# Optimization experiments

Measured on AMD Instinct MI355X. Metric: run time of the kernel, lower is better.

Reference implementation:

```python
import jax, jax.numpy as jnp
import numpy as np

S, B, H = 1024, 4096, 8  # seq_len, batch, hidden (=input) size


def setup_inputs() -> dict:
    key = jax.random.key(0)
    k0, k1, k2, k3, k4 = jax.random.split(key, 5)
    scale = 1.0 / np.sqrt(H)  # matches torch uniform(-1/sqrt(H), 1/sqrt(H)) magnitude
    return {
        "input_": jax.random.normal(k0, (S, B, H), dtype=jnp.float32),
        "w_ih": jax.random.uniform(k1, (3 * H, H), jnp.float32, -scale, scale),
        "w_hh": jax.random.uniform(k2, (3 * H, H), jnp.float32, -scale, scale),
        "b_ih": jax.random.uniform(k3, (3 * H,), jnp.float32, -scale, scale),
        "b_hh": jax.random.uniform(k4, (3 * H,), jnp.float32, -scale, scale),
    }


def _gru_seq(input_, w_ih, w_hh, b_ih, b_hh):
    # Precompute input-side gate projections for all timesteps in one GEMM:
    # (S, B, 3H); gate order in PyTorch GRU is r, z, n.
    xg = jnp.einsum("sbi,gi->sbg", input_, w_ih) + b_ih
    h0 = jnp.zeros((input_.shape[1], w_hh.shape[1]), dtype=input_.dtype)

    def step(h, xg_t):
        hg = h @ w_hh.T + b_hh                      # (B, 3H)
        xr, xz, xn = jnp.split(xg_t, 3, axis=-1)
        hr, hz, hn = jnp.split(hg, 3, axis=-1)
        r = jax.nn.sigmoid(xr + hr)
        z = jax.nn.sigmoid(xz + hz)
        n = jnp.tanh(xn + r * hn)
        h_new = (1.0 - z) * n + z * h
        return h_new, h_new

    h_last, outputs = jax.lax.scan(step, h0, xg)
    return outputs, h_last[None]  # (S, B, H), (1, B, H) like torch GRU


def reference(input_, w_ih, w_hh, b_ih, b_hh):
    return _gru_seq(input_, w_ih, w_hh, b_ih, b_hh)
```

## Files before the change

kernel.cpp:

```cpp
#include <hip/hip_runtime.h>

#define SS 1024
#define BB 4096
#define HH 8
#define XSTRIDE (BB * HH)

__device__ __forceinline__ int dpp_x1(int v) { return __builtin_amdgcn_mov_dpp(v, 0xB1, 0xF, 0xF, true); }
__device__ __forceinline__ int dpp_x2(int v) { return __builtin_amdgcn_mov_dpp(v, 0x4E, 0xF, 0xF, true); }
__device__ __forceinline__ int dpp_x3(int v) { return __builtin_amdgcn_mov_dpp(v, 0x1B, 0xF, 0xF, true); }
__device__ __forceinline__ int dpp_x7(int v) { return __builtin_amdgcn_mov_dpp(v, 0x141, 0xF, 0xF, true); }
__device__ __forceinline__ int dpp_r8(int v) { return __builtin_amdgcn_mov_dpp(v, 0x128, 0xF, 0xF, true); }

#define ALOADD(DST, PTR) asm volatile("global_load_dword %0, %1, off" : "=v"(DST) : "v"(PTR))

#define WAITV(N) do {                                                                  \
    asm volatile("s_waitcnt vmcnt(" #N ")" ::: "memory");                              \
    __builtin_amdgcn_sched_barrier(0);                                                 \
} while (0)

#define XFULL(BUF, V) do {                                                             \
    const float va = BUF[V];                                                           \
    const int vai = __float_as_int(va);                                                \
    const float vb = __int_as_float(dpp_x1(vai));                                      \
    const float vc = __int_as_float(dpp_x2(vai));                                      \
    const float vd = __int_as_float(dpp_x3(vai));                                      \
    float sr0 = fmaf(va, wri[0], bias_rx); sr0 = fmaf(vb, wri[1], sr0);                \
    float sr1 = vc * wri[2];               sr1 = fmaf(vd, wri[3], sr1);                \
    float sz0 = fmaf(va, wzi[0], bias_zx); sz0 = fmaf(vb, wzi[1], sz0);                \
    float sz1 = vc * wzi[2];               sz1 = fmaf(vd, wzi[3], sz1);                \
    float sn0 = fmaf(va, wni[0], bias_nx); sn0 = fmaf(vb, wni[1], sn0);                \
    float sn1 = vc * wni[2];               sn1 = fmaf(vd, wni[3], sn1);                \
    const float srt = sr0 + sr1, szt = sz0 + sz1, snt = sn0 + sn1;                     \
    xr[V] = srt + __int_as_float(dpp_r8(__float_as_int(srt)));                         \
    xz[V] = szt + __int_as_float(dpp_r8(__float_as_int(szt)));                         \
    xn[V] = snt + __int_as_float(dpp_r8(__float_as_int(snt)));                         \
} while (0)

#define GROUP(BUF, SBASE) do {                                                         \
    XFULL(BUF, 0);                                                                     \
    XFULL(BUF, 1);                                                                     \
    _Pragma("unroll")                                                                  \
    for (int u = 0; u < 8; ++u) {                                                      \
                                        \
        const int hvi = __float_as_int(hv);                                            \
        const float ha = hv;                                                           \
        const float hbv = __int_as_float(dpp_x1(hvi));                                 \
        const float hc = __int_as_float(dpp_x2(hvi));                                  \
        const float hd = __int_as_float(dpp_x3(hvi));                                  \
        float pr0 = ha * wrh[0];               pr0 = fmaf(hbv, wrh[1], pr0);           \
        float pr1 = hc * wrh[2];               pr1 = fmaf(hd, wrh[3], pr1);            \
        float pz0 = ha * wzh[0];               pz0 = fmaf(hbv, wzh[1], pz0);           \
        float pz1 = hc * wzh[2];               pz1 = fmaf(hd, wzh[3], pz1);            \
        float pn0 = fmaf(ha, wnh[0], bias_nh); pn0 = fmaf(hbv, wnh[1], pn0);           \
        float pn1 = hc * wnh[2];               pn1 = fmaf(hd, wnh[3], pn1);            \
        const float prt = pr0 + pr1, pzt = pz0 + pz1, pnt = pn0 + pn1;                 \
        const float srr = xr[u] + (prt + __int_as_float(dpp_r8(__float_as_int(prt)))); \
        const float szz = xz[u] + (pzt + __int_as_float(dpp_r8(__float_as_int(pzt)))); \
        const float snn = pnt + __int_as_float(dpp_r8(__float_as_int(pnt)));           \
        const bool W = (u + 2 < 8);                                                    \
        float wsr0, wsr1, wsz0, wsz1, wsn0, wsn1;                                      \
        float wvc, wvd;                                                                \
        if (W) {                    \
            const float va2 = BUF[u + 2];                                              \
            const int va2i = __float_as_int(va2);                                      \
            const float vb2 = __int_as_float(dpp_x1(va2i));                            \
            wvc = __int_as_float(dpp_x2(va2i));                                        \
            wvd = __int_as_float(dpp_x3(va2i));                                        \
            wsr0 = fmaf(va2, wri[0], bias_rx); wsr0 = fmaf(vb2, wri[1], wsr0);         \
            wsz0 = fmaf(va2, wzi[0], bias_zx); wsz0 = fmaf(vb2, wzi[1], wsz0);         \
            wsn0 = fmaf(va2, wni[0], bias_nx); wsn0 = fmaf(vb2, wni[1], wsn0);         \
        }                                                                              \
        const float er = __builtin_amdgcn_exp2f(srr);                                  \
        const float ez = __builtin_amdgcn_exp2f(szz);                                  \
        if (W) {                               \
            wsr1 = wvc * wri[2]; wsr1 = fmaf(wvd, wri[3], wsr1);                       \
            wsz1 = wvc * wzi[2]; wsz1 = fmaf(wvd, wzi[3], wsz1);                       \
            wsn1 = wvc * wni[2]; wsn1 = fmaf(wvd, wni[3], wsn1);                       \
        }                                                                              \
        const float r_ = __builtin_amdgcn_rcpf(1.0f + er);                             \
        const float z_ = __builtin_amdgcn_rcpf(1.0f + ez);                             \
        if (W) {                                  \
            const float srt = wsr0 + wsr1, szt = wsz0 + wsz1, snt = wsn0 + wsn1;       \
            xr[u + 2] = srt + __int_as_float(dpp_r8(__float_as_int(srt)));             \
            xz[u + 2] = szt + __int_as_float(dpp_r8(__float_as_int(szt)));             \
            xn[u + 2] = snt + __int_as_float(dpp_r8(__float_as_int(snt)));             \
        }                                                                              \
        const float en = __builtin_amdgcn_exp2f(fmaf(r_, snn, xn[u]));                 \
        const float n_ = fmaf(-2.0f, __builtin_amdgcn_rcpf(1.0f + en), 1.0f);          \
        h = n_ + z_ * (h - n_);                                                        \
            \
        const int hbits = __float_as_int(h);                                           \
        const int tA = dpp_x7(hbits);                                                  \
        const int tB = dpp_x3(tA);                                                     \
        hv = hiHalf ? __int_as_float(tB) : h;                                          \
                          \
        __builtin_nontemporal_store(h, &op[(size_t)((SBASE) + u) * XSTRIDE]);          \
    }                                                                                  \
} while (0)

#define LOADG(BUF, GRP) do {                                                           \
    const float* bp_ = xq + (size_t)(GRP) * 8 * XSTRIDE;                               \
    _Pragma("unroll")                                                                  \
    for (int u_ = 0; u_ < 8; ++u_) ALOADD(BUF[u_], bp_ + (size_t)u_ * XSTRIDE);        \
} while (0)

__global__ __launch_bounds__(64, 1) void gru_kernel(
    const float* __restrict__ x,
    const float* __restrict__ w_ih,
    const float* __restrict__ w_hh,
    const float* __restrict__ b_ih,
    const float* __restrict__ b_hh,
    float* __restrict__ out)
{
    const int lane = threadIdx.x;
    const int s16 = lane & 15;
    const int j = s16 & 7;
    const int half = s16 >> 3;
    const bool hiHalf = (half != 0);
    const int e0 = j ^ (half << 2);

    const float SR = -1.4426950408889634f;
    const float SN = 2.8853900817779268f;

    float wri[4], wzi[4], wni[4], wrh[4], wzh[4], wnh[4];
    #pragma unroll
    for (int m = 0; m < 4; ++m) {
        const int c = e0 ^ m;
        wri[m] = SR * w_ih[j * 8 + c];
        wzi[m] = SR * w_ih[(8 + j) * 8 + c];
        wni[m] = SN * w_ih[(16 + j) * 8 + c];
        wrh[m] = SR * w_hh[j * 8 + c];
        wzh[m] = SR * w_hh[(8 + j) * 8 + c];
        wnh[m] = SN * w_hh[(16 + j) * 8 + c];
    }
    const float bias_rx = hiHalf ? 0.0f : SR * (b_ih[j] + b_hh[j]);
    const float bias_zx = hiHalf ? 0.0f : SR * (b_ih[8 + j] + b_hh[8 + j]);
    const float bias_nx = hiHalf ? 0.0f : SN * b_ih[16 + j];
    const float bias_nh = hiHalf ? 0.0f : SN * b_hh[16 + j];

    const float* xq = x + (blockIdx.x << 5) + ((lane >> 4) << 3) + e0;
    float* op = out + (blockIdx.x << 5) + ((lane >> 4) << 3) + j;
    float* hlast = out + (size_t)SS * BB * HH + (blockIdx.x << 5) + ((lane >> 4) << 3) + j;

    float xA[8], xB[8];

    LOADG(xA, 0);
    LOADG(xB, 1);
    WAITV(8);

    float h = 0.0f;
    float hv = 0.0f;
    float xr[8], xz[8], xn[8];

    for (int g = 0; g < 124; g += 2) {
        GROUP(xA, g * 8);
        LOADG(xA, g + 2);
        WAITV(16);
        GROUP(xB, (g + 1) * 8);
        LOADG(xB, g + 3);
        WAITV(16);
    }
    GROUP(xA, 992);  LOADG(xA, 126); WAITV(16);
    GROUP(xB, 1000); LOADG(xB, 127); WAITV(16);
    GROUP(xA, 1008); WAITV(8);
    GROUP(xB, 1016);

    *hlast = h;
}

extern "C" void kernel_launch(void* const* d_in, const int* in_sizes, int n_in,
                              void* d_out, int out_size, void* d_ws, size_t ws_size,
                              hipStream_t stream) {
    const float* x    = (const float*)d_in[0];
    const float* w_ih = (const float*)d_in[1];
    const float* w_hh = (const float*)d_in[2];
    const float* b_ih = (const float*)d_in[3];
    const float* b_hh = (const float*)d_in[4];
    float* out = (float*)d_out;
    gru_kernel<<<BB / 4, 64, 0, stream>>>(x, w_ih, w_hh, b_ih, b_hh, out);
}
```

Before: 137.5 us.

## Split each batch row across 32 lanes to shorten per-step dependency chain

Each batch row's 8x8 matvec is now spread over 32 lanes (4 lanes per output, 2 inputs each) instead of 16 lanes with 4 inputs each. The partial sums are reduced with a DPP row shift plus a ds_swizzle, and the h broadcast is rebuilt for the four-way split. The grid doubles to 2048 blocks of 64 threads, and launch bounds now allow 2 waves per SIMD. This cuts FMAs on the serial recurrent path and adds occupancy, at the cost of twice as many waves and an LDS-latency swizzle in the critical chain.

```diff
diff --git a/kernel.cpp b/kernel.cpp
--- a/kernel.cpp
+++ b/kernel.cpp
@@ -11,6 +11,13 @@
 __device__ __forceinline__ int dpp_x7(int v) { return __builtin_amdgcn_mov_dpp(v, 0x141, 0xF, 0xF, true); }
 __device__ __forceinline__ int dpp_r8(int v) { return __builtin_amdgcn_mov_dpp(v, 0x128, 0xF, 0xF, true); }
 
+__device__ __forceinline__ float swz16(float v) {
+    return __int_as_float(__builtin_amdgcn_ds_swizzle(__float_as_int(v), 0x401F));
+}
+__device__ __forceinline__ float comb8(float p) {
+    return p + __int_as_float(dpp_r8(__float_as_int(p)));
+}
+
 #define ALOADD(DST, PTR) asm volatile("global_load_dword %0, %1, off" : "=v"(DST) : "v"(PTR))
 
 #define WAITV(N) do {                                                                  \
@@ -20,20 +27,14 @@
 
 #define XFULL(BUF, V) do {                                                             \
     const float va = BUF[V];                                                           \
-    const int vai = __float_as_int(va);                                                \
-    const float vb = __int_as_float(dpp_x1(vai));                                      \
-    const float vc = __int_as_float(dpp_x2(vai));                                      \
-    const float vd = __int_as_float(dpp_x3(vai));                                      \
-    float sr0 = fmaf(va, wri[0], bias_rx); sr0 = fmaf(vb, wri[1], sr0);                \
-    float sr1 = vc * wri[2];               sr1 = fmaf(vd, wri[3], sr1);                \
-    float sz0 = fmaf(va, wzi[0], bias_zx); sz0 = fmaf(vb, wzi[1], sz0);                \
-    float sz1 = vc * wzi[2];               sz1 = fmaf(vd, wzi[3], sz1);                \
-    float sn0 = fmaf(va, wni[0], bias_nx); sn0 = fmaf(vb, wni[1], sn0);                \
-    float sn1 = vc * wni[2];               sn1 = fmaf(vd, wni[3], sn1);                \
-    const float srt = sr0 + sr1, szt = sz0 + sz1, snt = sn0 + sn1;                     \
-    xr[V] = srt + __int_as_float(dpp_r8(__float_as_int(srt)));                         \
-    xz[V] = szt + __int_as_float(dpp_r8(__float_as_int(szt)));                         \
-    xn[V] = snt + __int_as_float(dpp_r8(__float_as_int(snt)));                         \
+    const float vb = __int_as_float(dpp_x1(__float_as_int(va)));                       \
+    float sr = fmaf(va, wri0, bias_rx); sr = fmaf(vb, wri1, sr);                       \
+    float sz = fmaf(va, wzi0, bias_zx); sz = fmaf(vb, wzi1, sz);                       \
+    float sn = fmaf(va, wni0, bias_nx); sn = fmaf(vb, wni1, sn);                       \
+    const float srp = comb8(sr), szp = comb8(sz), snp = comb8(sn);                     \
+    xr[V] = srp + swz16(srp);                                                          \
+    xz[V] = szp + swz16(szp);                                                          \
+    xn[V] = snp + swz16(snp);                                                          \
 } while (0)
 
 #define GROUP(BUF, SBASE) do {                                                         \
@@ -41,59 +42,47 @@
     XFULL(BUF, 1);                                                                     \
     _Pragma("unroll")                                                                  \
     for (int u = 0; u < 8; ++u) {                                                      \
-                                        \
-        const int hvi = __float_as_int(hv);                                            \
-        const float ha = hv;                                                           \
-        const float hbv = __int_as_float(dpp_x1(hvi));                                 \
-        const float hc = __int_as_float(dpp_x2(hvi));                                  \
-        const float hd = __int_as_float(dpp_x3(hvi));                                  \
-        float pr0 = ha * wrh[0];               pr0 = fmaf(hbv, wrh[1], pr0);           \
-        float pr1 = hc * wrh[2];               pr1 = fmaf(hd, wrh[3], pr1);            \
-        float pz0 = ha * wzh[0];               pz0 = fmaf(hbv, wzh[1], pz0);           \
-        float pz1 = hc * wzh[2];               pz1 = fmaf(hd, wzh[3], pz1);            \
-        float pn0 = fmaf(ha, wnh[0], bias_nh); pn0 = fmaf(hbv, wnh[1], pn0);           \
-        float pn1 = hc * wnh[2];               pn1 = fmaf(hd, wnh[3], pn1);            \
-        const float prt = pr0 + pr1, pzt = pz0 + pz1, pnt = pn0 + pn1;                 \
-        const float srr = xr[u] + (prt + __int_as_float(dpp_r8(__float_as_int(prt)))); \
-        const float szz = xz[u] + (pzt + __int_as_float(dpp_r8(__float_as_int(pzt)))); \
-        const float snn = pnt + __int_as_float(dpp_r8(__float_as_int(pnt)));           \
+                                         \
+        const float hb = __int_as_float(dpp_x1(__float_as_int(hv)));                   \
+        float pr = hv * wrh0;               pr = fmaf(hb, wrh1, pr);                   \
+        float pz = hv * wzh0;               pz = fmaf(hb, wzh1, pz);                   \
+        float pn = fmaf(hv, wnh0, bias_nh); pn = fmaf(hb, wnh1, pn);                   \
+        const float prp = comb8(pr), pzp = comb8(pz), pnp = comb8(pn);                 \
+        const float srr = xr[u] + (prp + swz16(prp));                                  \
+        const float szz = xz[u] + (pzp + swz16(pzp));                                  \
+        const float snn = pnp + swz16(pnp);                                            \
         const bool W = (u + 2 < 8);                                                    \
-        float wsr0, wsr1, wsz0, wsz1, wsn0, wsn1;                                      \
-        float wvc, wvd;                                                                \
-        if (W) {                    \
+        float wsr, wsz, wsn, wsrp, wszp, wsnp;                                         \
+        if (W) {                                      \
             const float va2 = BUF[u + 2];                                              \
-            const int va2i = __float_as_int(va2);                                      \
-            const float vb2 = __int_as_float(dpp_x1(va2i));                            \
-            wvc = __int_as_float(dpp_x2(va2i));                                        \
-            wvd = __int_as_float(dpp_x3(va2i));                                        \
-            wsr0 = fmaf(va2, wri[0], bias_rx); wsr0 = fmaf(vb2, wri[1], wsr0);         \
-            wsz0 = fmaf(va2, wzi[0], bias_zx); wsz0 = fmaf(vb2, wzi[1], wsz0);         \
-            wsn0 = fmaf(va2, wni[0], bias_nx); wsn0 = fmaf(vb2, wni[1], wsn0);         \
+            const float vb2 = __int_as_float(dpp_x1(__float_as_int(va2)));             \
+            wsr = fmaf(va2, wri0, bias_rx); wsr = fmaf(vb2, wri1, wsr);                \
+            wsz = fmaf(va2, wzi0, bias_zx); wsz = fmaf(vb2, wzi1, wsz);                \
+            wsn = fmaf(va2, wni0, bias_nx); wsn = fmaf(vb2, wni1, wsn);                \
         }                                                                              \
         const float er = __builtin_amdgcn_exp2f(srr);                                  \
         const float ez = __builtin_amdgcn_exp2f(szz);                                  \
-        if (W) {                               \
-            wsr1 = wvc * wri[2]; wsr1 = fmaf(wvd, wri[3], wsr1);                       \
-            wsz1 = wvc * wzi[2]; wsz1 = fmaf(wvd, wzi[3], wsz1);                       \
-            wsn1 = wvc * wni[2]; wsn1 = fmaf(wvd, wni[3], wsn1);                       \
+        if (W) {                                 \
+            wsrp = comb8(wsr); wszp = comb8(wsz); wsnp = comb8(wsn);                   \
         }                                                                              \
         const float r_ = __builtin_amdgcn_rcpf(1.0f + er);                             \
         const float z_ = __builtin_amdgcn_rcpf(1.0f + ez);                             \
-        if (W) {                                  \
-            const float srt = wsr0 + wsr1, szt = wsz0 + wsz1, snt = wsn0 + wsn1;       \
-            xr[u + 2] = srt + __int_as_float(dpp_r8(__float_as_int(srt)));             \
-            xz[u + 2] = szt + __int_as_float(dpp_r8(__float_as_int(szt)));             \
-            xn[u + 2] = snt + __int_as_float(dpp_r8(__float_as_int(snt)));             \
+        if (W) {                                    \
+            xr[u + 2] = wsrp + swz16(wsrp);                                            \
+            xz[u + 2] = wszp + swz16(wszp);                                            \
+            xn[u + 2] = wsnp + swz16(wsnp);                                            \
         }                                                                              \
         const float en = __builtin_amdgcn_exp2f(fmaf(r_, snn, xn[u]));                 \
         const float n_ = fmaf(-2.0f, __builtin_amdgcn_rcpf(1.0f + en), 1.0f);          \
         h = n_ + z_ * (h - n_);                                                        \
-            \
+         \
         const int hbits = __float_as_int(h);                                           \
-        const int tA = dpp_x7(hbits);                                                  \
-        const int tB = dpp_x3(tA);                                                     \
-        hv = hiHalf ? __int_as_float(tB) : h;                                          \
-                          \
+        const int t7 = dpp_x7(hbits);                                                  \
+        const float cb = __int_as_float(dpp_x2(hbits));                      \
+        const float cc = __int_as_float(dpp_x3(t7));                         \
+        const float cd = __int_as_float(dpp_x1(t7));                         \
+        hv = tHi ? (tOdd ? cd : cc) : (tOdd ? cb : h);                                 \
+                   \
         __builtin_nontemporal_store(h, &op[(size_t)((SBASE) + u) * XSTRIDE]);          \
     }                                                                                  \
 } while (0)
@@ -104,7 +93,7 @@
     for (int u_ = 0; u_ < 8; ++u_) ALOADD(BUF[u_], bp_ + (size_t)u_ * XSTRIDE);        \
 } while (0)
 
-__global__ __launch_bounds__(64, 1) void gru_kernel(
+__global__ __launch_bounds__(64, 2) void gru_kernel(
     const float* __restrict__ x,
     const float* __restrict__ w_ih,
     const float* __restrict__ w_hh,
@@ -113,34 +102,33 @@
     float* __restrict__ out)
 {
     const int lane = threadIdx.x;
-    const int s16 = lane & 15;
-    const int j = s16 & 7;
-    const int half = s16 >> 3;
-    const bool hiHalf = (half != 0);
-    const int e0 = j ^ (half << 2);
+    const int s32 = lane & 31;
+    const int j = s32 & 7;
+    const int t = s32 >> 3;
+    const int e0 = j ^ (t << 1);
+    const bool tOdd = (t & 1) != 0;
+    const bool tHi  = (t & 2) != 0;
 
     const float SR = -1.4426950408889634f;
     const float SN = 2.8853900817779268f;
 
-    float wri[4], wzi[4], wni[4], wrh[4], wzh[4], wnh[4];
-    #pragma unroll
-    for (int m = 0; m < 4; ++m) {
-        const int c = e0 ^ m;
-        wri[m] = SR * w_ih[j * 8 + c];
-        wzi[m] = SR * w_ih[(8 + j) * 8 + c];
-        wni[m] = SN * w_ih[(16 + j) * 8 + c];
-        wrh[m] = SR * w_hh[j * 8 + c];
-        wzh[m] = SR * w_hh[(8 + j) * 8 + c];
-        wnh[m] = SN * w_hh[(16 + j) * 8 + c];
-    }
-    const float bias_rx = hiHalf ? 0.0f : SR * (b_ih[j] + b_hh[j]);
-    const float bias_zx = hiHalf ? 0.0f : SR * (b_ih[8 + j] + b_hh[8 + j]);
-    const float bias_nx = hiHalf ? 0.0f : SN * b_ih[16 + j];
-    const float bias_nh = hiHalf ? 0.0f : SN * b_hh[16 + j];
+    const float wri0 = SR * w_ih[j * 8 + e0],        wri1 = SR * w_ih[j * 8 + (e0 ^ 1)];
+    const float wzi0 = SR * w_ih[(8 + j) * 8 + e0],  wzi1 = SR * w_ih[(8 + j) * 8 + (e0 ^ 1)];
+    const float wni0 = SN * w_ih[(16 + j) * 8 + e0], wni1 = SN * w_ih[(16 + j) * 8 + (e0 ^ 1)];
+    const float wrh0 = SR * w_hh[j * 8 + e0],        wrh1 = SR * w_hh[j * 8 + (e0 ^ 1)];
+    const float wzh0 = SR * w_hh[(8 + j) * 8 + e0],  wzh1 = SR * w_hh[(8 + j) * 8 + (e0 ^ 1)];
+    const float wnh0 = SN * w_hh[(16 + j) * 8 + e0], wnh1 = SN * w_hh[(16 + j) * 8 + (e0 ^ 1)];
 
-    const float* xq = x + (blockIdx.x << 5) + ((lane >> 4) << 3) + e0;
-    float* op = out + (blockIdx.x << 5) + ((lane >> 4) << 3) + j;
-    float* hlast = out + (size_t)SS * BB * HH + (blockIdx.x << 5) + ((lane >> 4) << 3) + j;
+    const bool t0lane = (t == 0);
+    const float bias_rx = t0lane ? SR * (b_ih[j] + b_hh[j]) : 0.0f;
+    const float bias_zx = t0lane ? SR * (b_ih[8 + j] + b_hh[8 + j]) : 0.0f;
+    const float bias_nx = t0lane ? SN * b_ih[16 + j] : 0.0f;
+    const float bias_nh = t0lane ? SN * b_hh[16 + j] : 0.0f;
+
+    const int bslice = (blockIdx.x << 4) + ((lane >> 5) << 3);
+    const float* xq = x + bslice + e0;
+    float* op = out + bslice + j;
+    float* hlast = out + (size_t)SS * BB * HH + bslice + j;
 
     float xA[8], xB[8];
 
@@ -177,5 +165,5 @@
     const float* b_ih = (const float*)d_in[3];
     const float* b_hh = (const float*)d_in[4];
     float* out = (float*)d_out;
-    gru_kernel<<<BB / 4, 64, 0, stream>>>(x, w_ih, w_hh, b_ih, b_hh, out);
+    gru_kernel<<<BB / 2, 64, 0, stream>>>(x, w_ih, w_hh, b_ih, b_hh, out);
 }
```

Result: slower. 248.9 us (+80.9%).
